# Kernel tuning notes

Hardware: AMD Instinct MI355X
Metric: run time of the kernel (lower is better)

The kernel has to match this reference:

```python
import jax, jax.numpy as jnp
import numpy as np

B, C, Hsp, Wsp = 16, 256, 64, 64
NUM_HEADS = 8
NORM_GROUPS = 4
EPS = 1e-5


def setup_inputs() -> dict:
    key = jax.random.key(0)
    ks = jax.random.split(key, 6)
    x = jax.random.normal(ks[0], (B, C, Hsp, Wsp), dtype=jnp.float32)
    gn_weight = jnp.ones((C,), dtype=jnp.float32)
    gn_bias = jnp.zeros((C,), dtype=jnp.float32)
    # Conv2d 1x1 kernels == dense matrices over channels
    qkv_weight = jax.random.normal(ks[1], (3 * C, C), dtype=jnp.float32) * (1.0 / np.sqrt(C))
    proj_weight = jax.random.normal(ks[2], (C, C), dtype=jnp.float32) * (1.0 / np.sqrt(C))
    proj_bias = jax.random.normal(ks[3], (C,), dtype=jnp.float32) * 0.01
    return {
        "x": x,
        "gn_weight": gn_weight,
        "gn_bias": gn_bias,
        "qkv_weight": qkv_weight,
        "proj_weight": proj_weight,
        "proj_bias": proj_bias,
    }


def reference(x, gn_weight, gn_bias, qkv_weight, proj_weight, proj_bias):
    b, c, h, w = x.shape
    hd = c // NUM_HEADS  # head dim
    n = h * w            # number of spatial tokens

    # GroupNorm over (c//G, h, w) per group, then per-channel affine
    xg = x.reshape(b, NORM_GROUPS, -1)
    mu = jnp.mean(xg, axis=-1, keepdims=True)
    var = jnp.mean(jnp.square(xg - mu), axis=-1, keepdims=True)
    xn = ((xg - mu) * jax.lax.rsqrt(var + EPS)).reshape(b, c, h, w)
    xn = xn * gn_weight[None, :, None, None] + gn_bias[None, :, None, None]

    # 1x1 conv (no bias) == channel matmul; output channel order matches torch view(b,3,H,d,h,w)
    qkv = jnp.einsum('bchw,oc->bohw', xn, qkv_weight)  # [b, 3c, h, w]
    qkv = qkv.reshape(b, 3, NUM_HEADS, hd, n)
    q, k, v = qkv[:, 0], qkv[:, 1], qkv[:, 2]          # each [b, H, d, n]

    # Linear (kernelized) attention: softmax over keys' token axis
    k = jax.nn.softmax(k, axis=-1)
    att = jnp.einsum('bhdn,bhen->bhde', k, v)          # [b, H, d, d]
    out = jnp.einsum('bhde,bhdn->bhen', att, q)        # [b, H, d, n]
    out = out.reshape(b, c, h, w)

    # Output 1x1 conv with bias
    return jnp.einsum('bchw,oc->bohw', out, proj_weight) + proj_bias[None, :, None, None]
```

## Files before the change

kernel.cpp:

```cpp
#include <hip/hip_runtime.h>
#include <hip/hip_bf16.h>


typedef __attribute__((ext_vector_type(4))) float f32x4;
typedef __attribute__((ext_vector_type(8))) short bf16x8;
typedef __attribute__((ext_vector_type(4))) short s16x4;
typedef __attribute__((ext_vector_type(8))) unsigned short u16x8;

__device__ inline float b2f(unsigned short u) {
  unsigned int x = ((unsigned int)u) << 16;
  float f; __builtin_memcpy(&f, &x, 4); return f;
}
__device__ inline unsigned short f2b(float f) {
  unsigned int x; __builtin_memcpy(&x, &f, 4);
  x += 0x7FFFu + ((x >> 16) & 1u);
  return (unsigned short)(x >> 16);
}

__global__ void __launch_bounds__(256) k_gn_partial(const float* __restrict__ x,
                                                    float* __restrict__ partials) {
  int blk = blockIdx.x;
  int grp = blk >> 4;
  int part = blk & 15;
  const float* base = x + (size_t)grp * 262144 + (size_t)part * 16384;
  int t = threadIdx.x;
  float s = 0.f, s2 = 0.f;
  for (int i = 0; i < 16; ++i) {
    f32x4 v = *(const f32x4*)(base + (size_t)(i * 256 + t) * 4);
    s  += v[0] + v[1] + v[2] + v[3];
    s2 += v[0]*v[0] + v[1]*v[1] + v[2]*v[2] + v[3]*v[3];
  }
  for (int o = 32; o > 0; o >>= 1) { s += __shfl_down(s, o); s2 += __shfl_down(s2, o); }
  __shared__ float ls[4], ls2[4];
  int w = t >> 6;
  if ((t & 63) == 0) { ls[w] = s; ls2[w] = s2; }
  __syncthreads();
  if (t == 0) {
    partials[blk * 2] = ls[0] + ls[1] + ls[2] + ls[3];
    partials[blk * 2 + 1] = ls2[0] + ls2[1] + ls2[2] + ls2[3];
  }
}

__global__ void __launch_bounds__(256) k_finalize(const float* __restrict__ partials,
                                                  float* __restrict__ stats,
                                                  const float* __restrict__ qkvw,
                                                  unsigned short* __restrict__ Wb,
                                                  unsigned short* __restrict__ WqT) {
  int bx = blockIdx.x, t = threadIdx.x;
  if (bx == 0) {
    if (t < 64) {
      float S = 0.f, S2 = 0.f;
      for (int i = 0; i < 16; ++i) { S += partials[(t * 16 + i) * 2]; S2 += partials[(t * 16 + i) * 2 + 1]; }
      float mu = S * (1.f / 262144.f);
      float var = S2 * (1.f / 262144.f) - mu * mu;
      stats[t * 2] = mu;
      stats[t * 2 + 1] = rsqrtf(var + 1e-5f);
    }
  } else if (bx <= 192) {
    int idx = (bx - 1) * 256 + t;
    f32x4 v = *(const f32x4*)(qkvw + (size_t)idx * 4);
    s16x4 o;
    for (int i = 0; i < 4; ++i) o[i] = (short)f2b(v[i]);
    *(s16x4*)(Wb + (size_t)idx * 4) = o;
  } else {
    int bb = bx - 193;
    int c = bb * 16 + (t & 15);
    int d0 = (t >> 4) * 16;
    for (int i = 0; i < 16; ++i) {
      int d = d0 + i;
      WqT[(size_t)c * 256 + d] = f2b(qkvw[(size_t)d * 256 + c]);
    }
  }
}

__global__ void __launch_bounds__(256) k_norm_t(const float* __restrict__ x,
                                                const float* __restrict__ stats,
                                                const float* __restrict__ gamma,
                                                const float* __restrict__ beta,
                                                unsigned short* __restrict__ xnT) {
  int blk = blockIdx.x;
  int b = blk >> 8;
  int tile = blk & 255;
  int ct = tile >> 6;
  int nt = tile & 63;
  int c0 = ct * 64, n0 = nt * 64;
  __shared__ float T[64][65];
  int t = threadIdx.x;
  float mu = stats[(b * 4 + ct) * 2];
  float rs = stats[(b * 4 + ct) * 2 + 1];
  int cl = t >> 2, q4 = t & 3;
  float sc = gamma[c0 + cl] * rs;
  float off = beta[c0 + cl] - mu * sc;
  const float* xr = x + ((size_t)b * 256 + c0 + cl) * 4096 + n0;
  for (int p = 0; p < 4; ++p) {
    int col = p * 16 + q4 * 4;
    f32x4 v = *(const f32x4*)(xr + col);
    for (int i = 0; i < 4; ++i) T[cl][col + i] = v[i] * sc + off;
  }
  __syncthreads();
  int nl = t >> 2, cc = t & 3;
  u16x8 o0, o1;
  for (int i = 0; i < 8; ++i) o0[i] = f2b(T[cc * 16 + i][nl]);
  for (int i = 0; i < 8; ++i) o1[i] = f2b(T[cc * 16 + 8 + i][nl]);
  unsigned short* dst = xnT + ((size_t)b * 4096 + n0 + nl) * 256 + c0 + cc * 16;
  *(u16x8*)dst = o0;
  *(u16x8*)(dst + 8) = o1;
}

__global__ void __launch_bounds__(256) k_attfused(const unsigned short* __restrict__ Wb,
                                                  const unsigned short* __restrict__ xnT,
                                                  float* __restrict__ attg,
                                                  float* __restrict__ rsums) {
  const int bx = blockIdx.x;
  const int b = bx >> 2, ns = bx & 3, h = blockIdx.y;
  const int hb = b * 8 + h;
  const int t = threadIdx.x;
  const int wave = t >> 6, lane = t & 63;
  const int g = lane >> 4, r = lane & 15;
  const int rh = wave >> 1;
  const int ch = wave & 1;
  __shared__ unsigned short PL[2][32][72];
  __shared__ unsigned short VL[2][32][72];

  const unsigned short* Wrow = Wb + (size_t)(256 + rh * 256 + h * 32) * 256;
  bf16x8 af[2][8];
#pragma unroll
  for (int rt = 0; rt < 2; ++rt)
#pragma unroll
    for (int kt = 0; kt < 8; ++kt)
      af[rt][kt] = *(const bf16x8*)(Wrow + (size_t)(rt * 16 + r) * 256 + kt * 32 + 8 * g);

  const unsigned short* Xb = xnT + ((size_t)b * 4096 + ns * 1024 + ch * 32 + r) * 256 + 8 * g;
  f32x4 attacc = {0.f, 0.f, 0.f, 0.f};
  float rs[2][4] = {{0.f,0.f,0.f,0.f},{0.f,0.f,0.f,0.f}};

  for (int c = 0; c < 16; ++c) {
    const int cur = c & 1;
    const unsigned short* Xc = Xb + (size_t)(c * 64) * 256;
    bf16x8 bfr[8][2];
#pragma unroll
    for (int kt = 0; kt < 8; ++kt)
#pragma unroll
      for (int ct = 0; ct < 2; ++ct)
        bfr[kt][ct] = *(const bf16x8*)(Xc + (size_t)(ct * 16) * 256 + kt * 32);
    f32x4 sacc[2][2] = {};
#pragma unroll
    for (int kt = 0; kt < 8; ++kt)
#pragma unroll
      for (int rt = 0; rt < 2; ++rt)
#pragma unroll
        for (int ct = 0; ct < 2; ++ct)
          sacc[rt][ct] = __builtin_amdgcn_mfma_f32_16x16x32_bf16(
              af[rt][kt], bfr[kt][ct], sacc[rt][ct], 0, 0, 0);
    if (rh == 0) {
#pragma unroll
      for (int rt = 0; rt < 2; ++rt)
#pragma unroll
        for (int ct = 0; ct < 2; ++ct)
#pragma unroll
          for (int reg = 0; reg < 4; ++reg) {
            float e = __expf(sacc[rt][ct][reg]);
            rs[rt][reg] += e;
            PL[cur][rt * 16 + 4 * g + reg][ch * 32 + ct * 16 + r] = f2b(e);
          }
    } else {
#pragma unroll
      for (int rt = 0; rt < 2; ++rt)
#pragma unroll
        for (int ct = 0; ct < 2; ++ct)
#pragma unroll
          for (int reg = 0; reg < 4; ++reg)
            VL[cur][rt * 16 + 4 * g + reg][ch * 32 + ct * 16 + r] = f2b(sacc[rt][ct][reg]);
    }
    __syncthreads();
#pragma unroll
    for (int ks = 0; ks < 2; ++ks) {
      bf16x8 pa = *(const bf16x8*)&PL[cur][rh * 16 + r][ks * 32 + 8 * g];
      bf16x8 vb = *(const bf16x8*)&VL[cur][ch * 16 + r][ks * 32 + 8 * g];
      attacc = __builtin_amdgcn_mfma_f32_16x16x32_bf16(pa, vb, attacc, 0, 0, 0);
    }
  }
  float* ab = attg + (size_t)hb * 1024;
#pragma unroll
  for (int reg = 0; reg < 4; ++reg)
    atomicAdd(&ab[(rh * 16 + 4 * g + reg) * 32 + ch * 16 + r], attacc[reg]);
  if (rh == 0) {
#pragma unroll
    for (int rt = 0; rt < 2; ++rt)
#pragma unroll
      for (int reg = 0; reg < 4; ++reg) {
        float v = rs[rt][reg];
        v += __shfl_xor(v, 1); v += __shfl_xor(v, 2);
        v += __shfl_xor(v, 4); v += __shfl_xor(v, 8);
        if (r == 0) atomicAdd(&rsums[hb * 32 + rt * 16 + 4 * g + reg], v);
      }
  }
}

template<bool OUT_BF16, bool ADD_BIAS>
__global__ void __launch_bounds__(256)
k_gemm_bt(const unsigned short* __restrict__ A,
          const unsigned short* __restrict__ B,
          void* __restrict__ Cv,
          const float* __restrict__ bias,
          long sA, long sB, long sC, int ldc) {
  __shared__ unsigned short LA[128][32];
  __shared__ unsigned short LB[128][32];
  const int t = threadIdx.x;
  const unsigned short* Ab = A + (size_t)blockIdx.z * sA + (size_t)blockIdx.x * 128 * 256;
  const unsigned short* Bb = B + (size_t)blockIdx.z * sB + (size_t)blockIdx.y * 128 * 256;
  const int wave = t >> 6, lane = t & 63;
  const int wm = wave >> 1, wn = wave & 1;
  const int g = lane >> 4, r = lane & 15;
  const int rA = t >> 2, sslot = t & 3;
  const int ws0 = 8 * (sslot ^ (rA & 3));
  const int rslot = 8 * (g ^ (r & 3));
  const unsigned short* ag = Ab + (size_t)rA * 256 + 8 * sslot;
  const unsigned short* bg = Bb + (size_t)rA * 256 + 8 * sslot;
  u16x8 pa0 = *(const u16x8*)(ag);
  u16x8 pa1 = *(const u16x8*)(ag + 64 * 256);
  u16x8 pb0 = *(const u16x8*)(bg);
  u16x8 pb1 = *(const u16x8*)(bg + 64 * 256);
  f32x4 acc[4][4] = {};
  for (int kt = 0; kt < 8; ++kt) {
    if (kt) __syncthreads();
    *(u16x8*)&LA[rA][ws0] = pa0;  *(u16x8*)&LA[rA + 64][ws0] = pa1;
    *(u16x8*)&LB[rA][ws0] = pb0;  *(u16x8*)&LB[rA + 64][ws0] = pb1;
    __syncthreads();
    if (kt < 7) {
      int off = (kt + 1) * 32;
      pa0 = *(const u16x8*)(ag + off);  pa1 = *(const u16x8*)(ag + 64 * 256 + off);
      pb0 = *(const u16x8*)(bg + off);  pb1 = *(const u16x8*)(bg + 64 * 256 + off);
    }
    bf16x8 af[4], bfr[4];
    for (int i = 0; i < 4; ++i) {
      af[i]  = *(const bf16x8*)&LA[wm * 64 + i * 16 + r][rslot];
      bfr[i] = *(const bf16x8*)&LB[wn * 64 + i * 16 + r][rslot];
    }
    for (int mi = 0; mi < 4; ++mi)
      for (int ni = 0; ni < 4; ++ni)
        acc[mi][ni] = __builtin_amdgcn_mfma_f32_16x16x32_bf16(af[mi], bfr[ni], acc[mi][ni], 0, 0, 0);
  }
  const int m0 = blockIdx.x * 128 + wm * 64;
  const int n0 = blockIdx.y * 128 + wn * 64;
  if (OUT_BF16) {
    unsigned short* C = (unsigned short*)Cv + (size_t)blockIdx.z * sC;
    for (int mi = 0; mi < 4; ++mi)
      for (int ni = 0; ni < 4; ++ni) {
        int row = m0 + mi * 16 + 4 * g;
        int col = n0 + ni * 16 + r;
        for (int reg = 0; reg < 4; ++reg)
          C[(size_t)(row + reg) * ldc + col] = f2b(acc[mi][ni][reg]);
      }
  } else {
    float* C = (float*)Cv + (size_t)blockIdx.z * sC;
    for (int mi = 0; mi < 4; ++mi)
      for (int ni = 0; ni < 4; ++ni) {
        int row = m0 + mi * 16 + 4 * g;
        int col = n0 + ni * 16 + r;
        for (int reg = 0; reg < 4; ++reg) {
          float v = acc[mi][ni][reg];
          if (ADD_BIAS) v += bias[row + reg];
          C[(size_t)(row + reg) * ldc + col] = v;
        }
      }
  }
}

__global__ void __launch_bounds__(256) k_makeM(const float* __restrict__ attg,
                                               const float* __restrict__ rsums,
                                               const float* __restrict__ projw,
                                               unsigned short* __restrict__ Mb) {
  int blk = blockIdx.x;
  int b = blk >> 3, h = blk & 7;
  __shared__ float attL[32][33];
  __shared__ float invs[32];
  int t = threadIdx.x;
  if (t < 32) invs[t] = 1.f / rsums[blk * 32 + t];
  const float* asrc = attg + (size_t)blk * 1024;
  {
    f32x4 v = *(const f32x4*)(asrc + (size_t)t * 4);
    int idx = t * 4;
    for (int i = 0; i < 4; ++i) attL[(idx + i) >> 5][(idx + i) & 31] = v[i];
  }
  __syncthreads();
  float pw[32];
  const float* ps = projw + (size_t)t * 256 + h * 32;
  for (int i = 0; i < 8; ++i) {
    f32x4 v = *(const f32x4*)(ps + i * 4);
    pw[i * 4 + 0] = v[0]; pw[i * 4 + 1] = v[1]; pw[i * 4 + 2] = v[2]; pw[i * 4 + 3] = v[3];
  }
  unsigned short* dst = Mb + ((size_t)b * 256 + t) * 256 + h * 32;
  for (int dd = 0; dd < 32; ++dd) {
    float s = 0.f;
    for (int e = 0; e < 32; ++e) s += pw[e] * attL[dd][e];
    dst[dd] = f2b(s * invs[dd]);
  }
}

__global__ void __launch_bounds__(256) k_gemm_final(const unsigned short* __restrict__ M2,
                                                    const unsigned short* __restrict__ xnT,
                                                    float* __restrict__ out,
                                                    const float* __restrict__ bias) {
  const int nt = blockIdx.x, b = blockIdx.y;
  const unsigned short* Ab = M2 + (size_t)b * 65536;
  const unsigned short* Bb = xnT + ((size_t)b * 4096 + nt * 64) * 256;
  float* Cb = out + (size_t)b * 1048576 + (size_t)nt * 64;
  __shared__ unsigned short LB[2][64][32];
  const int t = threadIdx.x;
  const int wave = t >> 6, lane = t & 63, g = lane >> 4, r = lane & 15;
  const int srow = t >> 2, sslot = t & 3;
  const int ws0 = 8 * (sslot ^ (srow & 3));
  const int rslot = 8 * (g ^ (r & 3));
  const unsigned short* bg = Bb + (size_t)srow * 256 + 8 * sslot;
  const unsigned short* ar = Ab + (size_t)(wave * 64 + r) * 256 + 8 * g;
  u16x8 pb = *(const u16x8*)bg;
  f32x4 acc[4][4] = {};
  for (int kt = 0; kt < 8; ++kt) {
    const int cur = kt & 1;
    *(u16x8*)&LB[cur][srow][ws0] = pb;
    __syncthreads();
    if (kt < 7) pb = *(const u16x8*)(bg + (kt + 1) * 32);
    bf16x8 af[4], bfr[4];
#pragma unroll
    for (int mi = 0; mi < 4; ++mi)
      af[mi] = *(const bf16x8*)(ar + (size_t)(mi * 16) * 256 + kt * 32);
#pragma unroll
    for (int ni = 0; ni < 4; ++ni)
      bfr[ni] = *(const bf16x8*)&LB[cur][ni * 16 + r][rslot];
#pragma unroll
    for (int mi = 0; mi < 4; ++mi)
#pragma unroll
      for (int ni = 0; ni < 4; ++ni)
        acc[mi][ni] = __builtin_amdgcn_mfma_f32_16x16x32_bf16(af[mi], bfr[ni], acc[mi][ni], 0, 0, 0);
  }
#pragma unroll
  for (int mi = 0; mi < 4; ++mi) {
    const int row = wave * 64 + mi * 16 + 4 * g;
#pragma unroll
    for (int ni = 0; ni < 4; ++ni)
#pragma unroll
      for (int reg = 0; reg < 4; ++reg)
        Cb[(size_t)(row + reg) * 4096 + ni * 16 + r] = acc[mi][ni][reg] + bias[row + reg];
  }
}

extern "C" void kernel_launch(void* const* d_in, const int* in_sizes, int n_in,
                              void* d_out, int out_size, void* d_ws, size_t ws_size,
                              hipStream_t stream) {
  (void)in_sizes; (void)n_in; (void)out_size; (void)ws_size;
  const float* x     = (const float*)d_in[0];
  const float* gn_w  = (const float*)d_in[1];
  const float* gn_b  = (const float*)d_in[2];
  const float* qkvw  = (const float*)d_in[3];
  const float* projw = (const float*)d_in[4];
  const float* projb = (const float*)d_in[5];

  char* ws = (char*)d_ws;
  float*          partials = (float*)(ws);
  float*          stats    = (float*)(ws + 8192);
  unsigned short* Wb       = (unsigned short*)(ws + 16384);
  unsigned short* Mb       = (unsigned short*)(ws + 409600);
  float*          attg     = (float*)(ws + 2506752);
  float*          rsums    = (float*)(ws + 3031040);
  unsigned short* WqT      = (unsigned short*)(ws + 3047424);
  unsigned short* M2       = (unsigned short*)(ws + 3178496);
  unsigned short* xnT      = (unsigned short*)(ws + 8388608);

  k_gn_partial<<<1024, 256, 0, stream>>>(x, partials);
  k_finalize<<<209, 256, 0, stream>>>(partials, stats, qkvw, Wb, WqT);
  k_norm_t<<<4096, 256, 0, stream>>>(x, stats, gn_w, gn_b, xnT);
  (void)hipMemsetAsync(attg, 0, 540672, stream);
  k_attfused<<<dim3(64, 8), 256, 0, stream>>>(Wb, xnT, attg, rsums);
  k_makeM<<<128, 256, 0, stream>>>(attg, rsums, projw, Mb);
  k_gemm_bt<true, false><<<dim3(2, 2, 16), 256, 0, stream>>>(
      Mb, WqT, (void*)M2, nullptr, 65536L, 0L, 65536L, 256);
  k_gemm_final<<<dim3(64, 16), 256, 0, stream>>>(M2, xnT, (float*)d_out, projb);
}
```

Measured before the change: 249.9 us.

## Software-pipeline xnT fragment loads across chunks in fused attention kernel

Loads the B fragments for the next chunk while computing MFMAs on the current chunk, using a register double-buffer, so global load latency overlaps with compute. It also raises wave priority around the MFMA block and adds a minimum-occupancy hint of 2 blocks per CU to launch bounds. The cost is more live registers (two sets of 16 bf16x8 fragments), which could cause spills under the tighter occupancy limit. The final iteration issues a redundant wraparound load of chunk 0.

After: 240.0 us. 4.0% less time.

```diff
diff --git a/kernel.cpp b/kernel.cpp
--- a/kernel.cpp
+++ b/kernel.cpp
@@ -107,10 +107,10 @@
   *(u16x8*)(dst + 8) = o1;
 }
 
-__global__ void __launch_bounds__(256) k_attfused(const unsigned short* __restrict__ Wb,
-                                                  const unsigned short* __restrict__ xnT,
-                                                  float* __restrict__ attg,
-                                                  float* __restrict__ rsums) {
+__global__ void __launch_bounds__(256, 2) k_attfused(const unsigned short* __restrict__ Wb,
+                                                     const unsigned short* __restrict__ xnT,
+                                                     float* __restrict__ attg,
+                                                     float* __restrict__ rsums) {
   const int bx = blockIdx.x;
   const int b = bx >> 2, ns = bx & 3, h = blockIdx.y;
   const int hb = b * 8 + h;
@@ -134,24 +134,29 @@
   f32x4 attacc = {0.f, 0.f, 0.f, 0.f};
   float rs[2][4] = {{0.f,0.f,0.f,0.f},{0.f,0.f,0.f,0.f}};
 
+  bf16x8 bfr[8][2];
+#pragma unroll
+  for (int kt = 0; kt < 8; ++kt) {
+    bfr[kt][0] = *(const bf16x8*)(Xb + kt * 32);
+    bfr[kt][1] = *(const bf16x8*)(Xb + (size_t)(16 * 256) + kt * 32);
+  }
+
   for (int c = 0; c < 16; ++c) {
     const int cur = c & 1;
-    const unsigned short* Xc = Xb + (size_t)(c * 64) * 256;
-    bf16x8 bfr[8][2];
-#pragma unroll
-    for (int kt = 0; kt < 8; ++kt)
-#pragma unroll
-      for (int ct = 0; ct < 2; ++ct)
-        bfr[kt][ct] = *(const bf16x8*)(Xc + (size_t)(ct * 16) * 256 + kt * 32);
+    const unsigned short* Xn = Xb + (size_t)(((c + 1) & 15) * 64) * 256;
     f32x4 sacc[2][2] = {};
-#pragma unroll
-    for (int kt = 0; kt < 8; ++kt)
-#pragma unroll
-      for (int rt = 0; rt < 2; ++rt)
-#pragma unroll
-        for (int ct = 0; ct < 2; ++ct)
-          sacc[rt][ct] = __builtin_amdgcn_mfma_f32_16x16x32_bf16(
-              af[rt][kt], bfr[kt][ct], sacc[rt][ct], 0, 0, 0);
+    __builtin_amdgcn_s_setprio(1);
+#pragma unroll
+    for (int kt = 0; kt < 8; ++kt) {
+      bf16x8 b0 = bfr[kt][0], b1 = bfr[kt][1];
+      bfr[kt][0] = *(const bf16x8*)(Xn + kt * 32);
+      bfr[kt][1] = *(const bf16x8*)(Xn + (size_t)(16 * 256) + kt * 32);
+      sacc[0][0] = __builtin_amdgcn_mfma_f32_16x16x32_bf16(af[0][kt], b0, sacc[0][0], 0, 0, 0);
+      sacc[0][1] = __builtin_amdgcn_mfma_f32_16x16x32_bf16(af[0][kt], b1, sacc[0][1], 0, 0, 0);
+      sacc[1][0] = __builtin_amdgcn_mfma_f32_16x16x32_bf16(af[1][kt], b0, sacc[1][0], 0, 0, 0);
+      sacc[1][1] = __builtin_amdgcn_mfma_f32_16x16x32_bf16(af[1][kt], b1, sacc[1][1], 0, 0, 0);
+    }
+    __builtin_amdgcn_s_setprio(0);
     if (rh == 0) {
 #pragma unroll
       for (int rt = 0; rt < 2; ++rt)
```
